# Optimization experiments

Measured on AMD Instinct MI355X. Metric: run time of the kernel, lower is better.

## Reference

```python
import jax, jax.numpy as jnp
import numpy as np

B, N, C = 512, 512, 96  # N = D*H*W with D=H=W=8


def _conv3d(x, w, b, groups=1):
    # x: [B, C, D, H, W], w: [O, I/groups, kd, kh, kw]
    y = jax.lax.conv_general_dilated(
        x, w, window_strides=(1, 1, 1), padding='SAME',
        dimension_numbers=('NCDHW', 'OIDHW', 'NCDHW'),
        feature_group_count=groups)
    return y + b[None, :, None, None, None]


def setup_inputs() -> dict:
    key = jax.random.key(0)
    ks = jax.random.split(key, 8)
    s1 = 0.1   # keep pre-softmax logits in a sane range
    sd = 0.2
    inp = {
        'x': jax.random.normal(ks[0], (B, N, C), jnp.float32),
        'wq1': jax.random.normal(ks[1], (C, C, 1, 1, 1), jnp.float32) * s1,
        'bq1': jnp.zeros((C,), jnp.float32),
        'wk1': jax.random.normal(ks[2], (C, C, 1, 1, 1), jnp.float32) * s1,
        'bk1': jnp.zeros((C,), jnp.float32),
        'wv1': jax.random.normal(ks[3], (C, C, 1, 1, 1), jnp.float32) * s1,
        'bv1': jnp.zeros((C,), jnp.float32),
        'wqd': jax.random.normal(ks[4], (C, 1, 3, 3, 3), jnp.float32) * sd,
        'bqd': jnp.zeros((C,), jnp.float32),
        'wkd': jax.random.normal(ks[5], (C, 1, 3, 3, 3), jnp.float32) * sd,
        'bkd': jnp.zeros((C,), jnp.float32),
        'wvd': jax.random.normal(ks[6], (C, 1, 3, 3, 3), jnp.float32) * sd,
        'bvd': jnp.zeros((C,), jnp.float32),
    }
    return inp


def reference(x, wq1, bq1, wk1, bk1, wv1, bv1, wqd, bqd, wkd, bkd, wvd, bvd):
    b, n, c = x.shape
    d = int(round(n ** (1.0 / 3.0)))
    # [B, N, C] -> [B, C, D, H, W]
    x5 = x.reshape(b, d, d, d, c).transpose(0, 4, 1, 2, 3)
    q = _conv3d(_conv3d(x5, wq1, bq1), wqd, bqd, groups=c)
    k = _conv3d(_conv3d(x5, wk1, bk1), wkd, bkd, groups=c)
    v = _conv3d(_conv3d(x5, wv1, bv1), wvd, bvd, groups=c)
    # [B, C, D, H, W] -> [B, N, C]
    q = q.transpose(0, 2, 3, 4, 1).reshape(b, n, c)
    k = k.transpose(0, 2, 3, 4, 1).reshape(b, n, c)
    v = v.transpose(0, 2, 3, 4, 1).reshape(b, n, c)
    attn = jnp.einsum('bnc,bmc->bnm', q, k) / jnp.sqrt(jnp.float32(c))
    attn = jax.nn.softmax(attn, axis=-1)
    out = jnp.einsum('bnm,bmc->bnc', attn, v)
    return out
```

## Files before the change

kernel.cpp:

```cpp
#include <hip/hip_runtime.h>
#include <math.h>

typedef _Float16 f16;
typedef _Float16 f16x2 __attribute__((ext_vector_type(2)));
typedef _Float16 f16x8 __attribute__((ext_vector_type(8)));
typedef __fp16 fp16x2 __attribute__((ext_vector_type(2)));
typedef float f32x4 __attribute__((ext_vector_type(4)));

union F2U { f16x2 h; fp16x2 p; unsigned u; };
union U2H { uint2 q; f16x2 h[2]; f16 f[4]; };
union U4H { uint4 q; f16x2 h[4]; f16 f[8]; };
union V8H { f16x8 v; f16x2 h[4]; f16 f[8]; };

__device__ __forceinline__ f16x2 uAsH(unsigned u) { F2U c; c.u = u; return c.h; }
__device__ __forceinline__ unsigned hAsU(f16x2 h) { F2U c; c.h = h; return c.u; }
__device__ __forceinline__ unsigned pAsU(fp16x2 p) { F2U c; c.p = p; return c.u; }

__device__ __forceinline__ f16x8 ld8cvt(const float* p) {
    float4 a = *(const float4*)p;
    float4 b = *(const float4*)(p + 4);
    V8H r;
    r.f[0] = (f16)a.x; r.f[1] = (f16)a.y; r.f[2] = (f16)a.z; r.f[3] = (f16)a.w;
    r.f[4] = (f16)b.x; r.f[5] = (f16)b.y; r.f[6] = (f16)b.z; r.f[7] = (f16)b.w;
    return r.v;
}

constexpr size_t PL = (size_t)512 * 512 * 96;

__global__ __launch_bounds__(512) void k12_fused(
    const float* __restrict__ x,
    const float* __restrict__ wq1, const float* __restrict__ bq1,
    const float* __restrict__ wk1, const float* __restrict__ bk1,
    const float* __restrict__ wv1, const float* __restrict__ bv1,
    const float* __restrict__ wqd, const float* __restrict__ bqd,
    const float* __restrict__ wkd, const float* __restrict__ bkd,
    const float* __restrict__ wvd, const float* __restrict__ bvd,
    f16* __restrict__ qo, f16* __restrict__ ko, f16* __restrict__ vo)
{
    __shared__ __align__(16) char sm[74400];

    const int tid = threadIdx.x;
    const int id = blockIdx.x;
    const int b = id / 6;
    const int r6 = id - b * 6;
    const int which = r6 >> 1;
    const int chalf = r6 & 1;
    const int ch0 = chalf * 48;
    const int wv_ = tid >> 6, lane = tid & 63, lr = lane & 15, lk = lane >> 4;

    const float* w1 = (which == 0) ? wq1 : ((which == 1) ? wk1 : wv1);
    const float* b1 = (which == 0) ? bq1 : ((which == 1) ? bk1 : bv1);
    const float* wd = (which == 0) ? wqd : ((which == 1) ? wkd : wvd);
    const float* bd = (which == 0) ? bqd : ((which == 1) ? bkd : bvd);
    const float* xb = x + (size_t)b * 512 * 96;

    if (which < 2) {
        f16*      slab = (f16*)sm;
        f16*      Wsh  = (f16*)(sm + 61440);
        unsigned* wdh  = (unsigned*)(sm + 71424);
        float*    bl1  = (float*)(sm + 74016);
        float*    bld  = (float*)(sm + 74208);

        #pragma unroll
        for (int it = 0; it < 3; ++it) {
            int g = tid + it * 512;
            if (g < 1152) {
                int i = g * 4;
                int co = i / 96, ci = i % 96;
                float4 v4 = *(const float4*)(w1 + (size_t)(ch0 + co) * 96 + ci);
                f16x2 h01 = { (f16)v4.x, (f16)v4.y };
                f16x2 h23 = { (f16)v4.z, (f16)v4.w };
                uint2 st; st.x = hAsU(h01); st.y = hAsU(h23);
                *(uint2*)(Wsh + co * 104 + ci) = st;
            }
        }
        for (int ii = tid; ii < 1296; ii += 512) {
            int lc = ii / 27, t2 = ii % 27;
            ((f16*)wdh)[t2 * 48 + lc] = (f16)wd[(ch0 + lc) * 27 + t2];
        }
        if (tid < 48) { bl1[tid] = b1[ch0 + tid]; bld[tid] = bd[ch0 + tid]; }
        __syncthreads();

        f32x4 acc[4][3];
        #pragma unroll
        for (int pg = 0; pg < 4; ++pg)
            #pragma unroll
            for (int cg = 0; cg < 3; ++cg) acc[pg][cg] = f32x4{0.f, 0.f, 0.f, 0.f};
        #pragma unroll
        for (int ks = 0; ks < 3; ++ks) {
            f16x8 bfr[3];
            #pragma unroll
            for (int cg = 0; cg < 3; ++cg)
                bfr[cg] = *(const f16x8*)(Wsh + (cg * 16 + lr) * 104 + ks * 32 + lk * 8);
            #pragma unroll
            for (int pg = 0; pg < 4; ++pg) {
                f16x8 a = ld8cvt(xb + (size_t)(wv_ * 64 + pg * 16 + lr) * 96 + ks * 32 + lk * 8);
                #pragma unroll
                for (int cg = 0; cg < 3; ++cg)
                    acc[pg][cg] = __builtin_amdgcn_mfma_f32_16x16x32_f16(bfr[cg], a, acc[pg][cg], 0, 0, 0);
            }
        }
        __syncthreads();

        #pragma unroll
        for (int pg = 0; pg < 4; ++pg) {
            int pos = wv_ * 64 + pg * 16 + lr;
            #pragma unroll
            for (int cg = 0; cg < 3; ++cg) {
                float4 bv4 = *(const float4*)&bl1[cg * 16 + lk * 4];
                f16x2 h01 = { (f16)(acc[pg][cg][0] + bv4.x), (f16)(acc[pg][cg][1] + bv4.y) };
                f16x2 h23 = { (f16)(acc[pg][cg][2] + bv4.z), (f16)(acc[pg][cg][3] + bv4.w) };
                uint2 st; st.x = hAsU(h01); st.y = hAsU(h23);
                *(uint2*)(slab + pos * 60 + cg * 16 + lk * 4) = st;
            }
        }
        __syncthreads();

        f16* outb = ((which == 0) ? qo : ko) + (size_t)b * 512 * 96;
        #pragma unroll
        for (int half = 0; half < 2; ++half) {
            if (half == 1 && tid >= 256) break;
            const int u = half * 512 + tid;
            const int r = u / 12;
            const int g4 = u - r * 12;
            const int dd = r >> 3, hh = r & 7;
            const int col = g4 * 4;
            float mo[8][4];
            {
                float4 b0 = *(const float4*)&bld[col];
                #pragma unroll
                for (int w = 0; w < 8; ++w) {
                    mo[w][0] = b0.x; mo[w][1] = b0.y; mo[w][2] = b0.z; mo[w][3] = b0.w;
                }
            }
            #pragma unroll
            for (int kd = 0; kd < 3; ++kd) {
                const int d2 = dd + kd - 1;
                const bool vd = (unsigned)d2 < 8u;
                f16x2 pa[8][2];
                #pragma unroll
                for (int w = 0; w < 8; ++w) {
                    pa[w][0] = f16x2{0, 0}; pa[w][1] = f16x2{0, 0};
                }
                #pragma unroll
                for (int kh = 0; kh < 3; ++kh) {
                    const int h2 = hh + kh - 1;
                    const unsigned vm = (vd && ((unsigned)h2 < 8u)) ? 0xFFFFFFFFu : 0u;
                    const int base = (vm ? (d2 * 64 + h2 * 8) : 0) * 60 + col;
                    U2H in[8];
                    #pragma unroll
                    for (int w2 = 0; w2 < 8; ++w2)
                        in[w2].q = *(const uint2*)(slab + base + w2 * 60);
                    const int t0 = (kd * 3 + kh) * 3;
                    f16x2 wt0[2], wt1[2], wt2[2];
                    #pragma unroll
                    for (int p = 0; p < 2; ++p) {
                        wt0[p] = uAsH(wdh[(t0 + 0) * 24 + g4 * 2 + p] & vm);
                        wt1[p] = uAsH(wdh[(t0 + 1) * 24 + g4 * 2 + p] & vm);
                        wt2[p] = uAsH(wdh[(t0 + 2) * 24 + g4 * 2 + p] & vm);
                    }
                    #pragma unroll
                    for (int w = 0; w < 8; ++w) {
                        #pragma unroll
                        for (int p = 0; p < 2; ++p) {
                            f16x2 s = pa[w][p];
                            s = in[w].h[p] * wt1[p] + s;
                            if (w > 0) s = in[w - 1].h[p] * wt0[p] + s;
                            if (w < 7) s = in[w + 1].h[p] * wt2[p] + s;
                            pa[w][p] = s;
                        }
                    }
                }
                #pragma unroll
                for (int w = 0; w < 8; ++w)
                    #pragma unroll
                    for (int p = 0; p < 2; ++p) {
                        mo[w][2 * p]     += (float)pa[w][p].x;
                        mo[w][2 * p + 1] += (float)pa[w][p].y;
                    }
            }
            #pragma unroll
            for (int w = 0; w < 8; ++w) {
                f16x2 h0 = { (f16)mo[w][0], (f16)mo[w][1] };
                f16x2 h1 = { (f16)mo[w][2], (f16)mo[w][3] };
                uint2 st; st.x = hAsU(h0); st.y = hAsU(h1);
                *(uint2*)(outb + (size_t)(r * 8 + w) * 96 + ch0 + col) = st;
            }
        }
    } else {
        f16*      Vsh = (f16*)sm;
        f16*      Wsh = (f16*)(sm + 49920);
        unsigned* wdp = (unsigned*)(sm + 59904);
        float*    bl1 = (float*)(sm + 65088);
        float*    bld = (float*)(sm + 65280);

        #pragma unroll
        for (int it = 0; it < 3; ++it) {
            int g = tid + it * 512;
            if (g < 1152) {
                int i = g * 4;
                int co = i / 96, ci = i % 96;
                float4 v4 = *(const float4*)(w1 + (size_t)(ch0 + co) * 96 + ci);
                f16x2 h01 = { (f16)v4.x, (f16)v4.y };
                f16x2 h23 = { (f16)v4.z, (f16)v4.w };
                uint2 st; st.x = hAsU(h01); st.y = hAsU(h23);
                *(uint2*)(Wsh + co * 104 + ci) = st;
            }
        }
        for (int ii = tid; ii < 1296; ii += 512) {
            int lc = ii / 27, t2 = ii % 27;
            f16 hh = (f16)wd[(ch0 + lc) * 27 + t2];
            f16x2 hp = { hh, hh };
            wdp[lc * 27 + t2] = hAsU(hp);
        }
        if (tid < 48) { bl1[tid] = b1[ch0 + tid]; bld[tid] = bd[ch0 + tid]; }
        __syncthreads();

        f32x4 acc[4][3];
        #pragma unroll
        for (int pg = 0; pg < 4; ++pg)
            #pragma unroll
            for (int cg = 0; cg < 3; ++cg) acc[pg][cg] = f32x4{0.f, 0.f, 0.f, 0.f};
        #pragma unroll
        for (int ks = 0; ks < 3; ++ks) {
            f16x8 bfr[3];
            #pragma unroll
            for (int cg = 0; cg < 3; ++cg)
                bfr[cg] = *(const f16x8*)(Wsh + (cg * 16 + lr) * 104 + ks * 32 + lk * 8);
            #pragma unroll
            for (int pg = 0; pg < 4; ++pg) {
                f16x8 a = ld8cvt(xb + (size_t)(wv_ * 64 + pg * 16 + lr) * 96 + ks * 32 + lk * 8);
                #pragma unroll
                for (int cg = 0; cg < 3; ++cg)
                    acc[pg][cg] = __builtin_amdgcn_mfma_f32_16x16x32_f16(a, bfr[cg], acc[pg][cg], 0, 0, 0);
            }
        }
        __syncthreads();

        #pragma unroll
        for (int pg = 0; pg < 4; ++pg) {
            int pos = wv_ * 64 + pg * 16 + lk * 4;
            #pragma unroll
            for (int cg = 0; cg < 3; ++cg) {
                float bv = bl1[cg * 16 + lr];
                int lc = cg * 16 + lr;
                f16x2 h01 = { (f16)(acc[pg][cg][0] + bv), (f16)(acc[pg][cg][1] + bv) };
                f16x2 h23 = { (f16)(acc[pg][cg][2] + bv), (f16)(acc[pg][cg][3] + bv) };
                uint2 st; st.x = hAsU(h01); st.y = hAsU(h23);
                *(uint2*)(Vsh + lc * 520 + pos) = st;
            }
        }
        __syncthreads();

        f16* outb = vo + (size_t)b * 96 * 512;
        #pragma unroll
        for (int j = 0; j < 6; ++j) {
            int u = tid + j * 512;
            int c = u >> 6, dh = u & 63;
            int dd = dh >> 3, hh2 = dh & 7;
            f16x2 A0[4], A1[4], A2[4];
            #pragma unroll
            for (int p = 0; p < 4; ++p) {
                A0[p] = f16x2{0, 0}; A1[p] = f16x2{0, 0}; A2[p] = f16x2{0, 0};
            }
            #pragma unroll
            for (int kd = 0; kd < 3; ++kd) {
                int d2 = dd + kd - 1;
                unsigned vd_ = ((unsigned)d2 < 8u) ? 0xFFFFFFFFu : 0u;
                #pragma unroll
                for (int kh = 0; kh < 3; ++kh) {
                    int h2 = hh2 + kh - 1;
                    unsigned vm = ((((unsigned)h2 < 8u) ? 0xFFFFFFFFu : 0u) & vd_);
                    int rowoff = vm ? ((d2 * 8 + h2) * 8) : 0;
                    uint4 rw = *(const uint4*)(Vsh + c * 520 + rowoff);
                    unsigned r0 = rw.x, r1 = rw.y, r2 = rw.z, r3 = rw.w;
                    unsigned ms0 = r0 << 16;
                    unsigned ms1 = (r1 << 16) | (r0 >> 16);
                    unsigned ms2 = (r2 << 16) | (r1 >> 16);
                    unsigned ms3 = (r3 << 16) | (r2 >> 16);
                    unsigned ms4 = r3 >> 16;
                    int t0 = kd * 9 + kh * 3;
                    f16x2 w0 = uAsH(wdp[c * 27 + t0]     & vm);
                    f16x2 w1 = uAsH(wdp[c * 27 + t0 + 1] & vm);
                    f16x2 w2 = uAsH(wdp[c * 27 + t0 + 2] & vm);
                    f16x2* acc2 = (kd == 0) ? A0 : ((kd == 1) ? A1 : A2);
                    acc2[0] = uAsH(ms0) * w0 + acc2[0];
                    acc2[1] = uAsH(ms1) * w0 + acc2[1];
                    acc2[2] = uAsH(ms2) * w0 + acc2[2];
                    acc2[3] = uAsH(ms3) * w0 + acc2[3];
                    acc2[0] = uAsH(r0) * w1 + acc2[0];
                    acc2[1] = uAsH(r1) * w1 + acc2[1];
                    acc2[2] = uAsH(r2) * w1 + acc2[2];
                    acc2[3] = uAsH(r3) * w1 + acc2[3];
                    acc2[0] = uAsH(ms1) * w2 + acc2[0];
                    acc2[1] = uAsH(ms2) * w2 + acc2[1];
                    acc2[2] = uAsH(ms3) * w2 + acc2[2];
                    acc2[3] = uAsH(ms4) * w2 + acc2[3];
                }
            }
            float bv = bld[c];
            unsigned ow[4];
            #pragma unroll
            for (int p = 0; p < 4; ++p) {
                float lo = (float)A0[p].x + (float)A1[p].x + (float)A2[p].x + bv;
                float hi = (float)A0[p].y + (float)A1[p].y + (float)A2[p].y + bv;
                f16x2 hp = { (f16)lo, (f16)hi };
                ow[p] = hAsU(hp);
            }
            *(uint4*)(outb + (size_t)(ch0 + c) * 512 + dh * 8) = make_uint4(ow[0], ow[1], ow[2], ow[3]);
        }
    }
}

__global__ __launch_bounds__(512) void k3_attn(
    const f16* __restrict__ qF, const f16* __restrict__ kF, const f16* __restrict__ vF,
    float* __restrict__ outp)
{
    __shared__ __align__(16) f16 Ksh[512 * 104];
    __shared__ __align__(16) f16 Psh[8 * 1152];

    const int tid = threadIdx.x;
    const int b = blockIdx.x;
    const int wv_ = tid >> 6, lane = tid & 63, lr = lane & 15, lk = lane >> 4;

    const f16* qg = qF + ((size_t)b * 512 + wv_ * 64) * 96;
    const f16* kg = kF + (size_t)b * 512 * 96;
    const f16* vg = vF + (size_t)b * 96 * 512;

    const float scl = 0.14724447f;

    #pragma unroll
    for (int it = 0; it < 12; ++it) {
        int i = tid * 8 + it * 4096;
        int r = i / 96, c = i % 96;
        *(uint4*)(Ksh + r * 104 + c) = *(const uint4*)(kg + i);
    }
    __syncthreads();

    float sum_p[4] = {0.f, 0.f, 0.f, 0.f};
    f32x4 accO[4][6];
    #pragma unroll
    for (int qg2 = 0; qg2 < 4; ++qg2)
        #pragma unroll
        for (int cg = 0; cg < 6; ++cg) accO[qg2][cg] = f32x4{0.f, 0.f, 0.f, 0.f};

    f16* psw = Psh + wv_ * 1152;
    uint2* psw2 = (uint2*)psw;

    for (int t = 0; t < 8; ++t) {
        f16x8 kf[3][4];
        #pragma unroll
        for (int ks3 = 0; ks3 < 3; ++ks3)
            #pragma unroll
            for (int f = 0; f < 4; ++f)
                kf[ks3][f] = *(const f16x8*)(Ksh + (t * 64 + f * 16 + lr) * 104 + ks3 * 32 + lk * 8);
        f16x8 vb[2][6];
        #pragma unroll
        for (int ks2 = 0; ks2 < 2; ++ks2)
            #pragma unroll
            for (int cg = 0; cg < 6; ++cg)
                vb[ks2][cg] = *(const f16x8*)(vg + (size_t)(cg * 16 + lr) * 512
                                                 + t * 64 + ks2 * 32 + lk * 8);
        #pragma unroll
        for (int qg2 = 0; qg2 < 4; ++qg2) {
            f16x8 qf3[3];
            #pragma unroll
            for (int ks3 = 0; ks3 < 3; ++ks3)
                qf3[ks3] = *(const f16x8*)(qg + (qg2 * 16 + lr) * 96 + ks3 * 32 + lk * 8);
            f32x4 sa[4];
            #pragma unroll
            for (int f = 0; f < 4; ++f) sa[f] = f32x4{0.f, 0.f, 0.f, 0.f};
            #pragma unroll
            for (int ks3 = 0; ks3 < 3; ++ks3)
                #pragma unroll
                for (int f = 0; f < 4; ++f)
                    sa[f] = __builtin_amdgcn_mfma_f32_16x16x32_f16(kf[ks3][f], qf3[ks3], sa[f], 0, 0, 0);
            #pragma unroll
            for (int f = 0; f < 4; ++f) {
                float e0 = __builtin_amdgcn_exp2f(sa[f][0] * scl);
                float e1 = __builtin_amdgcn_exp2f(sa[f][1] * scl);
                float e2 = __builtin_amdgcn_exp2f(sa[f][2] * scl);
                float e3 = __builtin_amdgcn_exp2f(sa[f][3] * scl);
                sum_p[qg2] += (e0 + e1) + (e2 + e3);
                uint2 pk;
                pk.x = pAsU(__builtin_amdgcn_cvt_pkrtz(e0, e1));
                pk.y = pAsU(__builtin_amdgcn_cvt_pkrtz(e2, e3));
                psw2[lr * 18 + f * 4 + lk] = pk;
            }
            #pragma unroll
            for (int ks2 = 0; ks2 < 2; ++ks2) {
                f16x8 pb = *(const f16x8*)(psw + lr * 72 + ks2 * 32 + lk * 8);
                #pragma unroll
                for (int cg = 0; cg < 6; ++cg)
                    accO[qg2][cg] = __builtin_amdgcn_mfma_f32_16x16x32_f16(
                        vb[ks2][cg], pb, accO[qg2][cg], 0, 0, 0);
            }
        }
    }
    #pragma unroll
    for (int qg2 = 0; qg2 < 4; ++qg2) {
        sum_p[qg2] += __shfl_xor(sum_p[qg2], 16);
        sum_p[qg2] += __shfl_xor(sum_p[qg2], 32);
    }

    #pragma unroll
    for (int qg2 = 0; qg2 < 4; ++qg2) {
        const float inv = 1.0f / sum_p[qg2];
        float* og = outp + ((size_t)b * 512 + wv_ * 64 + qg2 * 16 + lr) * 96;
        #pragma unroll
        for (int cg = 0; cg < 6; ++cg) {
            float4 o4 = make_float4(accO[qg2][cg][0] * inv, accO[qg2][cg][1] * inv,
                                    accO[qg2][cg][2] * inv, accO[qg2][cg][3] * inv);
            *(float4*)(og + cg * 16 + lk * 4) = o4;
        }
    }
}

extern "C" void kernel_launch(void* const* d_in, const int* in_sizes, int n_in,
                              void* d_out, int out_size, void* d_ws, size_t ws_size,
                              hipStream_t stream) {
    const float* x   = (const float*)d_in[0];
    const float* wq1 = (const float*)d_in[1];
    const float* bq1 = (const float*)d_in[2];
    const float* wk1 = (const float*)d_in[3];
    const float* bk1 = (const float*)d_in[4];
    const float* wv1 = (const float*)d_in[5];
    const float* bv1 = (const float*)d_in[6];
    const float* wqd = (const float*)d_in[7];
    const float* bqd = (const float*)d_in[8];
    const float* wkd = (const float*)d_in[9];
    const float* bkd = (const float*)d_in[10];
    const float* wvd = (const float*)d_in[11];
    const float* bvd = (const float*)d_in[12];

    f16* ws = (f16*)d_ws;
    f16* q = ws;
    f16* k = ws + PL;
    f16* v = ws + 2 * PL;

    k12_fused<<<3072, 512, 0, stream>>>(x, wq1, bq1, wk1, bk1, wv1, bv1,
                                        wqd, bqd, wkd, bkd, wvd, bvd, q, k, v);
    k3_attn<<<512, 512, 0, stream>>>(q, k, v, (float*)d_out);
}
```

Before: 258.4 us.

## Reuse x tile across Q/K/V projections in one block, loop over outputs

The fused projection-plus-depthwise-conv kernel now launches one block per (batch, channel-half) instead of one per (batch, which, channel-half). Each block loads and converts its x tile to fp16 registers once, then loops over the Q, K and V projections. The 1x1 weights are read straight from global memory into MFMA fragments instead of being staged in shared memory, which shrinks the shared-memory footprint. The goal is to cut the repeated global reads and conversions of x by a factor of three. In exchange there are fewer, longer blocks and more registers held per thread for the x fragments, which may lower occupancy.

```diff
diff --git a/kernel.cpp b/kernel.cpp
--- a/kernel.cpp
+++ b/kernel.cpp
@@ -37,277 +37,247 @@
     const float* __restrict__ wvd, const float* __restrict__ bvd,
     f16* __restrict__ qo, f16* __restrict__ ko, f16* __restrict__ vo)
 {
-    __shared__ __align__(16) char sm[74400];
+    __shared__ __align__(16) char sm[67008];
+    f16*      slab = (f16*)sm;
+    unsigned* wdx  = (unsigned*)(sm + 61440);
+    float*    bl1  = (float*)(sm + 66624);
+    float*    bld  = (float*)(sm + 66816);
 
     const int tid = threadIdx.x;
     const int id = blockIdx.x;
-    const int b = id / 6;
-    const int r6 = id - b * 6;
-    const int which = r6 >> 1;
-    const int chalf = r6 & 1;
+    const int b = id >> 1;
+    const int chalf = id & 1;
     const int ch0 = chalf * 48;
     const int wv_ = tid >> 6, lane = tid & 63, lr = lane & 15, lk = lane >> 4;
 
-    const float* w1 = (which == 0) ? wq1 : ((which == 1) ? wk1 : wv1);
-    const float* b1 = (which == 0) ? bq1 : ((which == 1) ? bk1 : bv1);
-    const float* wd = (which == 0) ? wqd : ((which == 1) ? wkd : wvd);
-    const float* bd = (which == 0) ? bqd : ((which == 1) ? bkd : bvd);
     const float* xb = x + (size_t)b * 512 * 96;
 
-    if (which < 2) {
-        f16*      slab = (f16*)sm;
-        f16*      Wsh  = (f16*)(sm + 61440);
-        unsigned* wdh  = (unsigned*)(sm + 71424);
-        float*    bl1  = (float*)(sm + 74016);
-        float*    bld  = (float*)(sm + 74208);
-
-        #pragma unroll
-        for (int it = 0; it < 3; ++it) {
-            int g = tid + it * 512;
-            if (g < 1152) {
-                int i = g * 4;
-                int co = i / 96, ci = i % 96;
-                float4 v4 = *(const float4*)(w1 + (size_t)(ch0 + co) * 96 + ci);
-                f16x2 h01 = { (f16)v4.x, (f16)v4.y };
-                f16x2 h23 = { (f16)v4.z, (f16)v4.w };
-                uint2 st; st.x = hAsU(h01); st.y = hAsU(h23);
-                *(uint2*)(Wsh + co * 104 + ci) = st;
-            }
-        }
-        for (int ii = tid; ii < 1296; ii += 512) {
-            int lc = ii / 27, t2 = ii % 27;
-            ((f16*)wdh)[t2 * 48 + lc] = (f16)wd[(ch0 + lc) * 27 + t2];
+    f16x8 xa[4][3];
+    #pragma unroll
+    for (int pg = 0; pg < 4; ++pg)
+        #pragma unroll
+        for (int ks = 0; ks < 3; ++ks)
+            xa[pg][ks] = ld8cvt(xb + (size_t)(wv_ * 64 + pg * 16 + lr) * 96 + ks * 32 + lk * 8);
+
+    for (int which = 0; which < 3; ++which) {
+        const float* w1 = (which == 0) ? wq1 : ((which == 1) ? wk1 : wv1);
+        const float* b1 = (which == 0) ? bq1 : ((which == 1) ? bk1 : bv1);
+        const float* wd = (which == 0) ? wqd : ((which == 1) ? wkd : wvd);
+        const float* bd = (which == 0) ? bqd : ((which == 1) ? bkd : bvd);
+
+        __syncthreads();
+
+        if (which < 2) {
+            for (int ii = tid; ii < 1296; ii += 512) {
+                int lc = ii / 27, t2 = ii % 27;
+                ((f16*)wdx)[t2 * 48 + lc] = (f16)wd[(ch0 + lc) * 27 + t2];
+            }
+        } else {
+            for (int ii = tid; ii < 1296; ii += 512) {
+                int lc = ii / 27, t2 = ii % 27;
+                f16 hh = (f16)wd[(ch0 + lc) * 27 + t2];
+                f16x2 hp = { hh, hh };
+                wdx[lc * 27 + t2] = hAsU(hp);
+            }
         }
         if (tid < 48) { bl1[tid] = b1[ch0 + tid]; bld[tid] = bd[ch0 + tid]; }
+
+        f32x4 acc[4][3];
+        #pragma unroll
+        for (int pg = 0; pg < 4; ++pg)
+            #pragma unroll
+            for (int cg = 0; cg < 3; ++cg) acc[pg][cg] = f32x4{0.f, 0.f, 0.f, 0.f};
+        if (which < 2) {
+            #pragma unroll
+            for (int ks = 0; ks < 3; ++ks) {
+                f16x8 bfr[3];
+                #pragma unroll
+                for (int cg = 0; cg < 3; ++cg)
+                    bfr[cg] = ld8cvt(w1 + (size_t)(ch0 + cg * 16 + lr) * 96 + ks * 32 + lk * 8);
+                #pragma unroll
+                for (int pg = 0; pg < 4; ++pg)
+                    #pragma unroll
+                    for (int cg = 0; cg < 3; ++cg)
+                        acc[pg][cg] = __builtin_amdgcn_mfma_f32_16x16x32_f16(bfr[cg], xa[pg][ks], acc[pg][cg], 0, 0, 0);
+            }
+        } else {
+            #pragma unroll
+            for (int ks = 0; ks < 3; ++ks) {
+                f16x8 bfr[3];
+                #pragma unroll
+                for (int cg = 0; cg < 3; ++cg)
+                    bfr[cg] = ld8cvt(w1 + (size_t)(ch0 + cg * 16 + lr) * 96 + ks * 32 + lk * 8);
+                #pragma unroll
+                for (int pg = 0; pg < 4; ++pg)
+                    #pragma unroll
+                    for (int cg = 0; cg < 3; ++cg)
+                        acc[pg][cg] = __builtin_amdgcn_mfma_f32_16x16x32_f16(xa[pg][ks], bfr[cg], acc[pg][cg], 0, 0, 0);
+            }
+        }
         __syncthreads();
 
-        f32x4 acc[4][3];
-        #pragma unroll
-        for (int pg = 0; pg < 4; ++pg)
-            #pragma unroll
-            for (int cg = 0; cg < 3; ++cg) acc[pg][cg] = f32x4{0.f, 0.f, 0.f, 0.f};
-        #pragma unroll
-        for (int ks = 0; ks < 3; ++ks) {
-            f16x8 bfr[3];
-            #pragma unroll
-            for (int cg = 0; cg < 3; ++cg)
-                bfr[cg] = *(const f16x8*)(Wsh + (cg * 16 + lr) * 104 + ks * 32 + lk * 8);
+        if (which < 2) {
             #pragma unroll
             for (int pg = 0; pg < 4; ++pg) {
-                f16x8 a = ld8cvt(xb + (size_t)(wv_ * 64 + pg * 16 + lr) * 96 + ks * 32 + lk * 8);
-                #pragma unroll
-                for (int cg = 0; cg < 3; ++cg)
-                    acc[pg][cg] = __builtin_amdgcn_mfma_f32_16x16x32_f16(bfr[cg], a, acc[pg][cg], 0, 0, 0);
+                int pos = wv_ * 64 + pg * 16 + lr;
+                #pragma unroll
+                for (int cg = 0; cg < 3; ++cg) {
+                    float4 bv4 = *(const float4*)&bl1[cg * 16 + lk * 4];
+                    f16x2 h01 = { (f16)(acc[pg][cg][0] + bv4.x), (f16)(acc[pg][cg][1] + bv4.y) };
+                    f16x2 h23 = { (f16)(acc[pg][cg][2] + bv4.z), (f16)(acc[pg][cg][3] + bv4.w) };
+                    uint2 st; st.x = hAsU(h01); st.y = hAsU(h23);
+                    *(uint2*)(slab + pos * 60 + cg * 16 + lk * 4) = st;
+                }
+            }
+        } else {
+            #pragma unroll
+            for (int pg = 0; pg < 4; ++pg) {
+                int pos = wv_ * 64 + pg * 16 + lk * 4;
+                #pragma unroll
+                for (int cg = 0; cg < 3; ++cg) {
+                    float bv = bl1[cg * 16 + lr];
+                    int lc = cg * 16 + lr;
+                    f16x2 h01 = { (f16)(acc[pg][cg][0] + bv), (f16)(acc[pg][cg][1] + bv) };
+                    f16x2 h23 = { (f16)(acc[pg][cg][2] + bv), (f16)(acc[pg][cg][3] + bv) };
+                    uint2 st; st.x = hAsU(h01); st.y = hAsU(h23);
+                    *(uint2*)(slab + lc * 520 + pos) = st;
+                }
             }
         }
         __syncthreads();
 
-        #pragma unroll
-        for (int pg = 0; pg < 4; ++pg) {
-            int pos = wv_ * 64 + pg * 16 + lr;
-            #pragma unroll
-            for (int cg = 0; cg < 3; ++cg) {
-                float4 bv4 = *(const float4*)&bl1[cg * 16 + lk * 4];
-                f16x2 h01 = { (f16)(acc[pg][cg][0] + bv4.x), (f16)(acc[pg][cg][1] + bv4.y) };
-                f16x2 h23 = { (f16)(acc[pg][cg][2] + bv4.z), (f16)(acc[pg][cg][3] + bv4.w) };
-                uint2 st; st.x = hAsU(h01); st.y = hAsU(h23);
-                *(uint2*)(slab + pos * 60 + cg * 16 + lk * 4) = st;
-            }
-        }
-        __syncthreads();
-
-        f16* outb = ((which == 0) ? qo : ko) + (size_t)b * 512 * 96;
-        #pragma unroll
-        for (int half = 0; half < 2; ++half) {
-            if (half == 1 && tid >= 256) break;
-            const int u = half * 512 + tid;
-            const int r = u / 12;
-            const int g4 = u - r * 12;
-            const int dd = r >> 3, hh = r & 7;
-            const int col = g4 * 4;
-            float mo[8][4];
-            {
-                float4 b0 = *(const float4*)&bld[col];
-                #pragma unroll
-                for (int w = 0; w < 8; ++w) {
-                    mo[w][0] = b0.x; mo[w][1] = b0.y; mo[w][2] = b0.z; mo[w][3] = b0.w;
-                }
-            }
-            #pragma unroll
-            for (int kd = 0; kd < 3; ++kd) {
-                const int d2 = dd + kd - 1;
-                const bool vd = (unsigned)d2 < 8u;
-                f16x2 pa[8][2];
-                #pragma unroll
-                for (int w = 0; w < 8; ++w) {
-                    pa[w][0] = f16x2{0, 0}; pa[w][1] = f16x2{0, 0};
-                }
-                #pragma unroll
-                for (int kh = 0; kh < 3; ++kh) {
-                    const int h2 = hh + kh - 1;
-                    const unsigned vm = (vd && ((unsigned)h2 < 8u)) ? 0xFFFFFFFFu : 0u;
-                    const int base = (vm ? (d2 * 64 + h2 * 8) : 0) * 60 + col;
-                    U2H in[8];
-                    #pragma unroll
-                    for (int w2 = 0; w2 < 8; ++w2)
-                        in[w2].q = *(const uint2*)(slab + base + w2 * 60);
-                    const int t0 = (kd * 3 + kh) * 3;
-                    f16x2 wt0[2], wt1[2], wt2[2];
-                    #pragma unroll
-                    for (int p = 0; p < 2; ++p) {
-                        wt0[p] = uAsH(wdh[(t0 + 0) * 24 + g4 * 2 + p] & vm);
-                        wt1[p] = uAsH(wdh[(t0 + 1) * 24 + g4 * 2 + p] & vm);
-                        wt2[p] = uAsH(wdh[(t0 + 2) * 24 + g4 * 2 + p] & vm);
+        if (which < 2) {
+            unsigned* wdh = wdx;
+            f16* outb = ((which == 0) ? qo : ko) + (size_t)b * 512 * 96;
+            #pragma unroll
+            for (int half = 0; half < 2; ++half) {
+                if (half == 1 && tid >= 256) break;
+                const int u = half * 512 + tid;
+                const int r = u / 12;
+                const int g4 = u - r * 12;
+                const int dd = r >> 3, hh = r & 7;
+                const int col = g4 * 4;
+                float mo[8][4];
+                {
+                    float4 b0 = *(const float4*)&bld[col];
+                    #pragma unroll
+                    for (int w = 0; w < 8; ++w) {
+                        mo[w][0] = b0.x; mo[w][1] = b0.y; mo[w][2] = b0.z; mo[w][3] = b0.w;
                     }
+                }
+                #pragma unroll
+                for (int kd = 0; kd < 3; ++kd) {
+                    const int d2 = dd + kd - 1;
+                    const bool vd = (unsigned)d2 < 8u;
+                    f16x2 pa[8][2];
                     #pragma unroll
                     for (int w = 0; w < 8; ++w) {
+                        pa[w][0] = f16x2{0, 0}; pa[w][1] = f16x2{0, 0};
+                    }
+                    #pragma unroll
+                    for (int kh = 0; kh < 3; ++kh) {
+                        const int h2 = hh + kh - 1;
+                        const unsigned vm = (vd && ((unsigned)h2 < 8u)) ? 0xFFFFFFFFu : 0u;
+                        const int base = (vm ? (d2 * 64 + h2 * 8) : 0) * 60 + col;
+                        U2H in[8];
+                        #pragma unroll
+                        for (int w2 = 0; w2 < 8; ++w2)
+                            in[w2].q = *(const uint2*)(slab + base + w2 * 60);
+                        const int t0 = (kd * 3 + kh) * 3;
+                        f16x2 wt0[2], wt1[2], wt2[2];
                         #pragma unroll
                         for (int p = 0; p < 2; ++p) {
-                            f16x2 s = pa[w][p];
-                            s = in[w].h[p] * wt1[p] + s;
-                            if (w > 0) s = in[w - 1].h[p] * wt0[p] + s;
-                            if (w < 7) s = in[w + 1].h[p] * wt2[p] + s;
-                            pa[w][p] = s;
+                            wt0[p] = uAsH(wdh[(t0 + 0) * 24 + g4 * 2 + p] & vm);
+                            wt1[p] = uAsH(wdh[(t0 + 1) * 24 + g4 * 2 + p] & vm);
+                            wt2[p] = uAsH(wdh[(t0 + 2) * 24 + g4 * 2 + p] & vm);
+                        }
+                        #pragma unroll
+                        for (int w = 0; w < 8; ++w) {
+                            #pragma unroll
+                            for (int p = 0; p < 2; ++p) {
+                                f16x2 s = pa[w][p];
+                                s = in[w].h[p] * wt1[p] + s;
+                                if (w > 0) s = in[w - 1].h[p] * wt0[p] + s;
+                                if (w < 7) s = in[w + 1].h[p] * wt2[p] + s;
+                                pa[w][p] = s;
+                            }
                         }
                     }
-                }
-                #pragma unroll
-                for (int w = 0; w < 8; ++w)
-                    #pragma unroll
-                    for (int p = 0; p < 2; ++p) {
-                        mo[w][2 * p]     += (float)pa[w][p].x;
-                        mo[w][2 * p + 1] += (float)pa[w][p].y;
+                    #pragma unroll
+                    for (int w = 0; w < 8; ++w)
+                        #pragma unroll
+                        for (int p = 0; p < 2; ++p) {
+                            mo[w][2 * p]     += (float)pa[w][p].x;
+                            mo[w][2 * p + 1] += (float)pa[w][p].y;
+                        }
+                }
+                #pragma unroll
+                for (int w = 0; w < 8; ++w) {
+                    f16x2 h0 = { (f16)mo[w][0], (f16)mo[w][1] };
+                    f16x2 h1 = { (f16)mo[w][2], (f16)mo[w][3] };
+                    uint2 st; st.x = hAsU(h0); st.y = hAsU(h1);
+                    *(uint2*)(outb + (size_t)(r * 8 + w) * 96 + ch0 + col) = st;
+                }
+            }
+        } else {
+            unsigned* wdp = wdx;
+            f16* outb = vo + (size_t)b * 96 * 512;
+            #pragma unroll
+            for (int j = 0; j < 6; ++j) {
+                int u = tid + j * 512;
+                int c = u >> 6, dh = u & 63;
+                int dd = dh >> 3, hh2 = dh & 7;
+                f16x2 A0[4], A1[4], A2[4];
+                #pragma unroll
+                for (int p = 0; p < 4; ++p) {
+                    A0[p] = f16x2{0, 0}; A1[p] = f16x2{0, 0}; A2[p] = f16x2{0, 0};
+                }
+                #pragma unroll
+                for (int kd = 0; kd < 3; ++kd) {
+                    int d2 = dd + kd - 1;
+                    unsigned vd_ = ((unsigned)d2 < 8u) ? 0xFFFFFFFFu : 0u;
+                    #pragma unroll
+                    for (int kh = 0; kh < 3; ++kh) {
+                        int h2 = hh2 + kh - 1;
+                        unsigned vm = ((((unsigned)h2 < 8u) ? 0xFFFFFFFFu : 0u) & vd_);
+                        int rowoff = vm ? ((d2 * 8 + h2) * 8) : 0;
+                        uint4 rw = *(const uint4*)(slab + c * 520 + rowoff);
+                        unsigned r0 = rw.x, r1 = rw.y, r2 = rw.z, r3 = rw.w;
+                        unsigned ms0 = r0 << 16;
+                        unsigned ms1 = (r1 << 16) | (r0 >> 16);
+                        unsigned ms2 = (r2 << 16) | (r1 >> 16);
+                        unsigned ms3 = (r3 << 16) | (r2 >> 16);
+                        unsigned ms4 = r3 >> 16;
+                        int t0 = kd * 9 + kh * 3;
+                        f16x2 w0 = uAsH(wdp[c * 27 + t0]     & vm);
+                        f16x2 w1 = uAsH(wdp[c * 27 + t0 + 1] & vm);
+                        f16x2 w2 = uAsH(wdp[c * 27 + t0 + 2] & vm);
+                        f16x2* acc2 = (kd == 0) ? A0 : ((kd == 1) ? A1 : A2);
+                        acc2[0] = uAsH(ms0) * w0 + acc2[0];
+                        acc2[1] = uAsH(ms1) * w0 + acc2[1];
+                        acc2[2] = uAsH(ms2) * w0 + acc2[2];
+                        acc2[3] = uAsH(ms3) * w0 + acc2[3];
+                        acc2[0] = uAsH(r0) * w1 + acc2[0];
+                        acc2[1] = uAsH(r1) * w1 + acc2[1];
+                        acc2[2] = uAsH(r2) * w1 + acc2[2];
+                        acc2[3] = uAsH(r3) * w1 + acc2[3];
+                        acc2[0] = uAsH(ms1) * w2 + acc2[0];
+                        acc2[1] = uAsH(ms2) * w2 + acc2[1];
+                        acc2[2] = uAsH(ms3) * w2 + acc2[2];
+                        acc2[3] = uAsH(ms4) * w2 + acc2[3];
                     }
-            }
-            #pragma unroll
-            for (int w = 0; w < 8; ++w) {
-                f16x2 h0 = { (f16)mo[w][0], (f16)mo[w][1] };
-                f16x2 h1 = { (f16)mo[w][2], (f16)mo[w][3] };
-                uint2 st; st.x = hAsU(h0); st.y = hAsU(h1);
-                *(uint2*)(outb + (size_t)(r * 8 + w) * 96 + ch0 + col) = st;
-            }
-        }
-    } else {
-        f16*      Vsh = (f16*)sm;
-        f16*      Wsh = (f16*)(sm + 49920);
-        unsigned* wdp = (unsigned*)(sm + 59904);
-        float*    bl1 = (float*)(sm + 65088);
-        float*    bld = (float*)(sm + 65280);
-
-        #pragma unroll
-        for (int it = 0; it < 3; ++it) {
-            int g = tid + it * 512;
-            if (g < 1152) {
-                int i = g * 4;
-                int co = i / 96, ci = i % 96;
-                float4 v4 = *(const float4*)(w1 + (size_t)(ch0 + co) * 96 + ci);
-                f16x2 h01 = { (f16)v4.x, (f16)v4.y };
-                f16x2 h23 = { (f16)v4.z, (f16)v4.w };
-                uint2 st; st.x = hAsU(h01); st.y = hAsU(h23);
-                *(uint2*)(Wsh + co * 104 + ci) = st;
-            }
-        }
-        for (int ii = tid; ii < 1296; ii += 512) {
-            int lc = ii / 27, t2 = ii % 27;
-            f16 hh = (f16)wd[(ch0 + lc) * 27 + t2];
-            f16x2 hp = { hh, hh };
-            wdp[lc * 27 + t2] = hAsU(hp);
-        }
-        if (tid < 48) { bl1[tid] = b1[ch0 + tid]; bld[tid] = bd[ch0 + tid]; }
-        __syncthreads();
-
-        f32x4 acc[4][3];
-        #pragma unroll
-        for (int pg = 0; pg < 4; ++pg)
-            #pragma unroll
-            for (int cg = 0; cg < 3; ++cg) acc[pg][cg] = f32x4{0.f, 0.f, 0.f, 0.f};
-        #pragma unroll
-        for (int ks = 0; ks < 3; ++ks) {
-            f16x8 bfr[3];
-            #pragma unroll
-            for (int cg = 0; cg < 3; ++cg)
-                bfr[cg] = *(const f16x8*)(Wsh + (cg * 16 + lr) * 104 + ks * 32 + lk * 8);
-            #pragma unroll
-            for (int pg = 0; pg < 4; ++pg) {
-                f16x8 a = ld8cvt(xb + (size_t)(wv_ * 64 + pg * 16 + lr) * 96 + ks * 32 + lk * 8);
-                #pragma unroll
-                for (int cg = 0; cg < 3; ++cg)
-                    acc[pg][cg] = __builtin_amdgcn_mfma_f32_16x16x32_f16(a, bfr[cg], acc[pg][cg], 0, 0, 0);
-            }
-        }
-        __syncthreads();
-
-        #pragma unroll
-        for (int pg = 0; pg < 4; ++pg) {
-            int pos = wv_ * 64 + pg * 16 + lk * 4;
-            #pragma unroll
-            for (int cg = 0; cg < 3; ++cg) {
-                float bv = bl1[cg * 16 + lr];
-                int lc = cg * 16 + lr;
-                f16x2 h01 = { (f16)(acc[pg][cg][0] + bv), (f16)(acc[pg][cg][1] + bv) };
-                f16x2 h23 = { (f16)(acc[pg][cg][2] + bv), (f16)(acc[pg][cg][3] + bv) };
-                uint2 st; st.x = hAsU(h01); st.y = hAsU(h23);
-                *(uint2*)(Vsh + lc * 520 + pos) = st;
-            }
-        }
-        __syncthreads();
-
-        f16* outb = vo + (size_t)b * 96 * 512;
-        #pragma unroll
-        for (int j = 0; j < 6; ++j) {
-            int u = tid + j * 512;
-            int c = u >> 6, dh = u & 63;
-            int dd = dh >> 3, hh2 = dh & 7;
-            f16x2 A0[4], A1[4], A2[4];
-            #pragma unroll
-            for (int p = 0; p < 4; ++p) {
-                A0[p] = f16x2{0, 0}; A1[p] = f16x2{0, 0}; A2[p] = f16x2{0, 0};
-            }
-            #pragma unroll
-            for (int kd = 0; kd < 3; ++kd) {
-                int d2 = dd + kd - 1;
-                unsigned vd_ = ((unsigned)d2 < 8u) ? 0xFFFFFFFFu : 0u;
-                #pragma unroll
-                for (int kh = 0; kh < 3; ++kh) {
-                    int h2 = hh2 + kh - 1;
-                    unsigned vm = ((((unsigned)h2 < 8u) ? 0xFFFFFFFFu : 0u) & vd_);
-                    int rowoff = vm ? ((d2 * 8 + h2) * 8) : 0;
-                    uint4 rw = *(const uint4*)(Vsh + c * 520 + rowoff);
-                    unsigned r0 = rw.x, r1 = rw.y, r2 = rw.z, r3 = rw.w;
-                    unsigned ms0 = r0 << 16;
-                    unsigned ms1 = (r1 << 16) | (r0 >> 16);
-                    unsigned ms2 = (r2 << 16) | (r1 >> 16);
-                    unsigned ms3 = (r3 << 16) | (r2 >> 16);
-                    unsigned ms4 = r3 >> 16;
-                    int t0 = kd * 9 + kh * 3;
-                    f16x2 w0 = uAsH(wdp[c * 27 + t0]     & vm);
-                    f16x2 w1 = uAsH(wdp[c * 27 + t0 + 1] & vm);
-                    f16x2 w2 = uAsH(wdp[c * 27 + t0 + 2] & vm);
-                    f16x2* acc2 = (kd == 0) ? A0 : ((kd == 1) ? A1 : A2);
-                    acc2[0] = uAsH(ms0) * w0 + acc2[0];
-                    acc2[1] = uAsH(ms1) * w0 + acc2[1];
-                    acc2[2] = uAsH(ms2) * w0 + acc2[2];
-                    acc2[3] = uAsH(ms3) * w0 + acc2[3];
-                    acc2[0] = uAsH(r0) * w1 + acc2[0];
-                    acc2[1] = uAsH(r1) * w1 + acc2[1];
-                    acc2[2] = uAsH(r2) * w1 + acc2[2];
-                    acc2[3] = uAsH(r3) * w1 + acc2[3];
-                    acc2[0] = uAsH(ms1) * w2 + acc2[0];
-                    acc2[1] = uAsH(ms2) * w2 + acc2[1];
-                    acc2[2] = uAsH(ms3) * w2 + acc2[2];
-                    acc2[3] = uAsH(ms4) * w2 + acc2[3];
-                }
-            }
-            float bv = bld[c];
-            unsigned ow[4];
-            #pragma unroll
-            for (int p = 0; p < 4; ++p) {
-                float lo = (float)A0[p].x + (float)A1[p].x + (float)A2[p].x + bv;
-                float hi = (float)A0[p].y + (float)A1[p].y + (float)A2[p].y + bv;
-                f16x2 hp = { (f16)lo, (f16)hi };
-                ow[p] = hAsU(hp);
-            }
-            *(uint4*)(outb + (size_t)(ch0 + c) * 512 + dh * 8) = make_uint4(ow[0], ow[1], ow[2], ow[3]);
+                }
+                float bv = bld[c];
+                unsigned ow[4];
+                #pragma unroll
+                for (int p = 0; p < 4; ++p) {
+                    float lo = (float)A0[p].x + (float)A1[p].x + (float)A2[p].x + bv;
+                    float hi = (float)A0[p].y + (float)A1[p].y + (float)A2[p].y + bv;
+                    f16x2 hp = { (f16)lo, (f16)hi };
+                    ow[p] = hAsU(hp);
+                }
+                *(uint4*)(outb + (size_t)(ch0 + c) * 512 + dh * 8) = make_uint4(ow[0], ow[1], ow[2], ow[3]);
+            }
         }
     }
 }
@@ -438,7 +408,7 @@
     f16* k = ws + PL;
     f16* v = ws + 2 * PL;
 
-    k12_fused<<<3072, 512, 0, stream>>>(x, wq1, bq1, wk1, bk1, wv1, bv1,
+    k12_fused<<<1024, 512, 0, stream>>>(x, wq1, bq1, wk1, bk1, wv1, bv1,
                                         wqd, bqd, wkd, bkd, wvd, bvd, q, k, v);
     k3_attn<<<512, 512, 0, stream>>>(q, k, v, (float*)d_out);
 }
```

After: 289.2 us. +11.9%, slower.
